# Kernel tuning notes

Measured on AMD Instinct MI355X. Metric: run time of the kernel, lower is better.

Reference implementation:

```python
import jax, jax.numpy as jnp
import numpy as np

B, T, D_Q, D_K, D_W = 128, 4096, 16, 16, 32


def setup_inputs() -> dict:
    key0 = jax.random.key(0)
    ks = jax.random.split(key0, 8)
    return {
        "query": jax.random.normal(ks[0], (B, 1, D_Q), dtype=jnp.float32),
        "key": jax.random.normal(ks[1], (B, T, D_K), dtype=jnp.float32),
        "value": jax.random.normal(ks[2], (B, T, D_K), dtype=jnp.float32),
        "W1": jax.random.normal(ks[3], (D_W, D_Q), dtype=jnp.float32) * 0.1,
        "W2": jax.random.normal(ks[4], (D_W, D_K), dtype=jnp.float32) * 0.1,
        "bias": jax.random.uniform(ks[5], (), dtype=jnp.float32, minval=-0.1, maxval=0.1),
        "v_w": jax.random.normal(ks[6], (1, D_W), dtype=jnp.float32) * 0.1,
        "v_b": jax.random.normal(ks[7], (1,), dtype=jnp.float32) * 0.1,
    }


def reference(query, key, value, W1, W2, bias, v_w, v_b):
    # Bahdanau additive attention.
    # query: [B,1,d_q], key/value: [B,T,d_k]
    q_proj = jnp.einsum('bqd,wd->bqw', query, W1)      # [B,1,d_w]
    k_proj = jnp.einsum('btd,wd->btw', key, W2)        # [B,T,d_w]
    h = jnp.tanh(k_proj + q_proj + bias)               # [B,T,d_w]
    score = (jnp.einsum('btw,ow->bto', h, v_w) + v_b).squeeze(-1)  # [B,T]
    attn = jax.nn.softmax(score, axis=-1)              # [B,T]
    context = jnp.einsum('bt,btd->bd', attn, value)[:, None, :]    # [B,1,d_v]
    return context, attn
```

## Files before the change

### kernel.cpp

```cpp
#include <hip/hip_runtime.h>

#define NB 128
#define NT 4096
#define DKD 16
#define DW 32
#define CHUNKS 8
#define TC 512
#define BLK 256
#define PT 2

__device__ __forceinline__ float fast_tanh(float x) {
    float e = __expf(2.0f * x);
    return 1.0f - 2.0f * __builtin_amdgcn_rcpf(e + 1.0f);
}

__global__ __launch_bounds__(BLK, 4) void aa_score(
    const float* __restrict__ query, const float* __restrict__ key,
    const float* __restrict__ value, const float* __restrict__ W1,
    const float* __restrict__ W2, const float* __restrict__ bias,
    const float* __restrict__ v_w, const float* __restrict__ v_b,
    float* __restrict__ attn,
    float* __restrict__ ws_l,
    float* __restrict__ ws_ctx)
{
    const int b   = blockIdx.x >> 3;
    const int c   = blockIdx.x & (CHUNKS - 1);
    const int tid = threadIdx.x;

    __shared__ float s_w2[DW * DKD];
    __shared__ float s_comb[DW];
    __shared__ float s_vw[DW];
    __shared__ float s_rctx[4 * 16];
    __shared__ float s_rl[4];

    if (tid < 128)
        reinterpret_cast<float4*>(s_w2)[tid] = reinterpret_cast<const float4*>(W2)[tid];
    if (tid >= 128 && tid < 128 + DW) {
        const int w = tid - 128;
        float acc = bias[0];
        const float* q  = query + b * DKD;
        const float* w1 = W1 + w * DKD;
        #pragma unroll
        for (int d = 0; d < DKD; ++d) acc = fmaf(q[d], w1[d], acc);
        s_comb[w] = acc;
        s_vw[w]   = v_w[w];
    }
    __syncthreads();

    const float vb = v_b[0];
    const size_t tbase = (size_t)b * NT + (size_t)c * TC + (size_t)tid * PT;
    const float4* kp = reinterpret_cast<const float4*>(key)   + tbase * 4;
    const float4* vp = reinterpret_cast<const float4*>(value) + tbase * 4;

    float4 k0[PT], k1[PT], k2[PT], k3[PT];
    float4 v0[PT], v1[PT], v2[PT], v3[PT];
    #pragma unroll
    for (int j = 0; j < PT; ++j) {
        k0[j] = kp[4*j + 0]; k1[j] = kp[4*j + 1];
        k2[j] = kp[4*j + 2]; k3[j] = kp[4*j + 3];
    }
    #pragma unroll
    for (int j = 0; j < PT; ++j) {
        v0[j] = vp[4*j + 0]; v1[j] = vp[4*j + 1];
        v2[j] = vp[4*j + 2]; v3[j] = vp[4*j + 3];
    }

    float sc[PT];
    #pragma unroll
    for (int j = 0; j < PT; ++j) sc[j] = vb;

    #pragma unroll 4
    for (int w = 0; w < DW; ++w) {
        const float4* wr = reinterpret_cast<const float4*>(s_w2 + w * DKD);
        const float4 w0 = wr[0], w1 = wr[1], w2 = wr[2], w3 = wr[3];
        const float cw = s_comb[w];
        const float vw = s_vw[w];
        #pragma unroll
        for (int j = 0; j < PT; ++j) {
            float h = cw;
            h = fmaf(k0[j].x, w0.x, h); h = fmaf(k0[j].y, w0.y, h);
            h = fmaf(k0[j].z, w0.z, h); h = fmaf(k0[j].w, w0.w, h);
            h = fmaf(k1[j].x, w1.x, h); h = fmaf(k1[j].y, w1.y, h);
            h = fmaf(k1[j].z, w1.z, h); h = fmaf(k1[j].w, w1.w, h);
            h = fmaf(k2[j].x, w2.x, h); h = fmaf(k2[j].y, w2.y, h);
            h = fmaf(k2[j].z, w2.z, h); h = fmaf(k2[j].w, w2.w, h);
            h = fmaf(k3[j].x, w3.x, h); h = fmaf(k3[j].y, w3.y, h);
            h = fmaf(k3[j].z, w3.z, h); h = fmaf(k3[j].w, w3.w, h);
            sc[j] = fmaf(fast_tanh(h), vw, sc[j]);
        }
    }

    float l = 0.0f;
    float ctx[16];
    #pragma unroll
    for (int d = 0; d < 16; ++d) ctx[d] = 0.0f;

    float p[PT];
    #pragma unroll
    for (int j = 0; j < PT; ++j) {
        p[j] = __expf(sc[j]);
        l += p[j];
        ctx[ 0] = fmaf(p[j], v0[j].x, ctx[ 0]); ctx[ 1] = fmaf(p[j], v0[j].y, ctx[ 1]);
        ctx[ 2] = fmaf(p[j], v0[j].z, ctx[ 2]); ctx[ 3] = fmaf(p[j], v0[j].w, ctx[ 3]);
        ctx[ 4] = fmaf(p[j], v1[j].x, ctx[ 4]); ctx[ 5] = fmaf(p[j], v1[j].y, ctx[ 5]);
        ctx[ 6] = fmaf(p[j], v1[j].z, ctx[ 6]); ctx[ 7] = fmaf(p[j], v1[j].w, ctx[ 7]);
        ctx[ 8] = fmaf(p[j], v2[j].x, ctx[ 8]); ctx[ 9] = fmaf(p[j], v2[j].y, ctx[ 9]);
        ctx[10] = fmaf(p[j], v2[j].z, ctx[10]); ctx[11] = fmaf(p[j], v2[j].w, ctx[11]);
        ctx[12] = fmaf(p[j], v3[j].x, ctx[12]); ctx[13] = fmaf(p[j], v3[j].y, ctx[13]);
        ctx[14] = fmaf(p[j], v3[j].z, ctx[14]); ctx[15] = fmaf(p[j], v3[j].w, ctx[15]);
    }

    reinterpret_cast<float2*>(attn + (size_t)b * NT + (size_t)c * TC)[tid] =
        make_float2(p[0], p[1]);

    #pragma unroll
    for (int o = 32; o > 0; o >>= 1) l += __shfl_xor(l, o);
    #pragma unroll
    for (int d = 0; d < 16; ++d) {
        #pragma unroll
        for (int o = 32; o > 0; o >>= 1) ctx[d] += __shfl_xor(ctx[d], o);
    }
    const int wave = tid >> 6;
    const int lane = tid & 63;
    if (lane == 0) {
        s_rl[wave] = l;
        #pragma unroll
        for (int d = 0; d < 16; ++d) s_rctx[wave * 16 + d] = ctx[d];
    }
    __syncthreads();
    const int slot = b * CHUNKS + c;
    if (tid < 16)
        ws_ctx[slot * 16 + tid] =
            s_rctx[tid] + s_rctx[16 + tid] + s_rctx[32 + tid] + s_rctx[48 + tid];
    if (tid == 0)
        ws_l[slot] = s_rl[0] + s_rl[1] + s_rl[2] + s_rl[3];
}

__global__ __launch_bounds__(BLK) void aa_finish(
    float* __restrict__ out,
    const float* __restrict__ ws_l,
    const float* __restrict__ ws_ctx)
{
    const int b   = blockIdx.x >> 3;
    const int c   = blockIdx.x & (CHUNKS - 1);
    const int tid = threadIdx.x;

    float L = 0.0f;
    #pragma unroll
    for (int i = 0; i < CHUNKS; ++i) L += ws_l[b * CHUNKS + i];
    const float inv = 1.0f / L;

    float2* ap = reinterpret_cast<float2*>(out + NB*DKD + (size_t)b * NT + (size_t)c * TC);
    float2 p = ap[tid];
    p.x *= inv; p.y *= inv;
    ap[tid] = p;

    if (c == 0 && tid < DKD) {
        const float* wc = ws_ctx + b * CHUNKS * 16;
        float s = 0.0f;
        #pragma unroll
        for (int i = 0; i < CHUNKS; ++i) s += wc[i * 16 + tid];
        out[b * DKD + tid] = s * inv;
    }
}

extern "C" void kernel_launch(void* const* d_in, const int* in_sizes, int n_in,
                              void* d_out, int out_size, void* d_ws, size_t ws_size,
                              hipStream_t stream) {
    const float* query = (const float*)d_in[0];
    const float* key   = (const float*)d_in[1];
    const float* value = (const float*)d_in[2];
    const float* W1    = (const float*)d_in[3];
    const float* W2    = (const float*)d_in[4];
    const float* bias  = (const float*)d_in[5];
    const float* v_w   = (const float*)d_in[6];
    const float* v_b   = (const float*)d_in[7];
    float* out = (float*)d_out;

    float* ws_l   = (float*)d_ws;
    float* ws_ctx = ws_l + NB * CHUNKS;

    aa_score<<<NB * CHUNKS, BLK, 0, stream>>>(
        query, key, value, W1, W2, bias, v_w, v_b,
        out + NB * DKD, ws_l, ws_ctx);
    aa_finish<<<NB * CHUNKS, BLK, 0, stream>>>(out, ws_l, ws_ctx);
}
```

Baseline: 117.4 us.

## Double per-thread work, read W2 from global, vectorize attn writes

```diff
diff --git a/kernel.cpp b/kernel.cpp
--- a/kernel.cpp
+++ b/kernel.cpp
@@ -4,17 +4,17 @@
 #define NT 4096
 #define DKD 16
 #define DW 32
-#define CHUNKS 8
-#define TC 512
+#define CHUNKS 4
+#define TC 1024
 #define BLK 256
-#define PT 2
+#define PT 4
 
 __device__ __forceinline__ float fast_tanh(float x) {
     float e = __expf(2.0f * x);
     return 1.0f - 2.0f * __builtin_amdgcn_rcpf(e + 1.0f);
 }
 
-__global__ __launch_bounds__(BLK, 4) void aa_score(
+__global__ __launch_bounds__(BLK, 2) void aa_score(
     const float* __restrict__ query, const float* __restrict__ key,
     const float* __restrict__ value, const float* __restrict__ W1,
     const float* __restrict__ W2, const float* __restrict__ bias,
@@ -23,27 +23,21 @@
     float* __restrict__ ws_l,
     float* __restrict__ ws_ctx)
 {
-    const int b   = blockIdx.x >> 3;
+    const int b   = blockIdx.x >> 2;
     const int c   = blockIdx.x & (CHUNKS - 1);
     const int tid = threadIdx.x;
 
-    __shared__ float s_w2[DW * DKD];
-    __shared__ float s_comb[DW];
-    __shared__ float s_vw[DW];
+    __shared__ float2 s_cv[DW];
     __shared__ float s_rctx[4 * 16];
     __shared__ float s_rl[4];
 
-    if (tid < 128)
-        reinterpret_cast<float4*>(s_w2)[tid] = reinterpret_cast<const float4*>(W2)[tid];
-    if (tid >= 128 && tid < 128 + DW) {
-        const int w = tid - 128;
+    if (tid < DW) {
         float acc = bias[0];
         const float* q  = query + b * DKD;
-        const float* w1 = W1 + w * DKD;
+        const float* wr = W1 + tid * DKD;
         #pragma unroll
-        for (int d = 0; d < DKD; ++d) acc = fmaf(q[d], w1[d], acc);
-        s_comb[w] = acc;
-        s_vw[w]   = v_w[w];
+        for (int d = 0; d < DKD; ++d) acc = fmaf(q[d], wr[d], acc);
+        s_cv[tid] = make_float2(acc, v_w[tid]);
     }
     __syncthreads();
 
@@ -71,22 +65,21 @@
 
     #pragma unroll 4
     for (int w = 0; w < DW; ++w) {
-        const float4* wr = reinterpret_cast<const float4*>(s_w2 + w * DKD);
-        const float4 w0 = wr[0], w1 = wr[1], w2 = wr[2], w3 = wr[3];
-        const float cw = s_comb[w];
-        const float vw = s_vw[w];
+        const float4* wrow = reinterpret_cast<const float4*>(W2 + w * DKD);
+        const float4 u0 = wrow[0], u1 = wrow[1], u2 = wrow[2], u3 = wrow[3];
+        const float2 cv = s_cv[w];
         #pragma unroll
         for (int j = 0; j < PT; ++j) {
-            float h = cw;
-            h = fmaf(k0[j].x, w0.x, h); h = fmaf(k0[j].y, w0.y, h);
-            h = fmaf(k0[j].z, w0.z, h); h = fmaf(k0[j].w, w0.w, h);
-            h = fmaf(k1[j].x, w1.x, h); h = fmaf(k1[j].y, w1.y, h);
-            h = fmaf(k1[j].z, w1.z, h); h = fmaf(k1[j].w, w1.w, h);
-            h = fmaf(k2[j].x, w2.x, h); h = fmaf(k2[j].y, w2.y, h);
-            h = fmaf(k2[j].z, w2.z, h); h = fmaf(k2[j].w, w2.w, h);
-            h = fmaf(k3[j].x, w3.x, h); h = fmaf(k3[j].y, w3.y, h);
-            h = fmaf(k3[j].z, w3.z, h); h = fmaf(k3[j].w, w3.w, h);
-            sc[j] = fmaf(fast_tanh(h), vw, sc[j]);
+            float h = cv.x;
+            h = fmaf(k0[j].x, u0.x, h); h = fmaf(k0[j].y, u0.y, h);
+            h = fmaf(k0[j].z, u0.z, h); h = fmaf(k0[j].w, u0.w, h);
+            h = fmaf(k1[j].x, u1.x, h); h = fmaf(k1[j].y, u1.y, h);
+            h = fmaf(k1[j].z, u1.z, h); h = fmaf(k1[j].w, u1.w, h);
+            h = fmaf(k2[j].x, u2.x, h); h = fmaf(k2[j].y, u2.y, h);
+            h = fmaf(k2[j].z, u2.z, h); h = fmaf(k2[j].w, u2.w, h);
+            h = fmaf(k3[j].x, u3.x, h); h = fmaf(k3[j].y, u3.y, h);
+            h = fmaf(k3[j].z, u3.z, h); h = fmaf(k3[j].w, u3.w, h);
+            sc[j] = fmaf(fast_tanh(h), cv.y, sc[j]);
         }
     }
 
@@ -110,8 +103,8 @@
         ctx[14] = fmaf(p[j], v3[j].z, ctx[14]); ctx[15] = fmaf(p[j], v3[j].w, ctx[15]);
     }
 
-    reinterpret_cast<float2*>(attn + (size_t)b * NT + (size_t)c * TC)[tid] =
-        make_float2(p[0], p[1]);
+    reinterpret_cast<float4*>(attn + (size_t)b * NT + (size_t)c * TC)[tid] =
+        make_float4(p[0], p[1], p[2], p[3]);
 
     #pragma unroll
     for (int o = 32; o > 0; o >>= 1) l += __shfl_xor(l, o);
@@ -141,8 +134,8 @@
     const float* __restrict__ ws_l,
     const float* __restrict__ ws_ctx)
 {
-    const int b   = blockIdx.x >> 3;
-    const int c   = blockIdx.x & (CHUNKS - 1);
+    const int b   = blockIdx.x >> 2;
+    const int q   = blockIdx.x & 3;
     const int tid = threadIdx.x;
 
     float L = 0.0f;
@@ -150,12 +143,13 @@
     for (int i = 0; i < CHUNKS; ++i) L += ws_l[b * CHUNKS + i];
     const float inv = 1.0f / L;
 
-    float2* ap = reinterpret_cast<float2*>(out + NB*DKD + (size_t)b * NT + (size_t)c * TC);
-    float2 p = ap[tid];
-    p.x *= inv; p.y *= inv;
-    ap[tid] = p;
+    float4* ap = reinterpret_cast<float4*>(out + NB * DKD + (size_t)b * NT) +
+                 q * BLK + tid;
+    float4 p = *ap;
+    p.x *= inv; p.y *= inv; p.z *= inv; p.w *= inv;
+    *ap = p;
 
-    if (c == 0 && tid < DKD) {
+    if (q == 0 && tid < DKD) {
         const float* wc = ws_ctx + b * CHUNKS * 16;
         float s = 0.0f;
         #pragma unroll
@@ -183,5 +177,5 @@
     aa_score<<<NB * CHUNKS, BLK, 0, stream>>>(
         query, key, value, W1, W2, bias, v_w, v_b,
         out + NB * DKD, ws_l, ws_ctx);
-    aa_finish<<<NB * CHUNKS, BLK, 0, stream>>>(out, ws_l, ws_ctx);
+    aa_finish<<<NB * (NT / 4 / BLK), BLK, 0, stream>>>(out, ws_l, ws_ctx);
 }
```

New measurement: 122.0 us. +3.9%, slower.
